# Performance work log

Measured on AMD Instinct MI355X. Metric: run time of the kernel, lower is better.

## Reference

```python
import jax, jax.numpy as jnp
import numpy as np

L, D, H, V, BS = 12, 768, 12, 50257, 1024  # n_layer, n_embd, n_head, vocab, block_size
B, T = 2, 1024
HD = D // H
SCALE = HD ** -0.5


def setup_inputs() -> dict:
    key = jax.random.key(0)
    ks = jax.random.split(key, 10)
    s = 0.02  # init std from _init_weights
    f = lambda k, shape: jax.random.normal(k, shape, jnp.float32) * s
    return {
        "idx": jax.random.randint(ks[0], (B, T), 0, V),
        "tok_emb": f(ks[1], (V, D)),          # tied with LM head
        "pos_emb": f(ks[2], (BS, D)),
        "wqkv": f(ks[3], (L, 3 * D, D)), "bqkv": jnp.zeros((L, 3 * D), jnp.float32),
        "wproj": f(ks[4], (L, D, D)),    "bproj": jnp.zeros((L, D), jnp.float32),
        "ln1_g": jnp.ones((L, D), jnp.float32), "ln1_b": jnp.zeros((L, D), jnp.float32),
        "ln2_g": jnp.ones((L, D), jnp.float32), "ln2_b": jnp.zeros((L, D), jnp.float32),
        "w1": f(ks[5], (L, 4 * D, D)), "b1": jnp.zeros((L, 4 * D), jnp.float32),
        "w2": f(ks[6], (L, D, 4 * D)), "b2": jnp.zeros((L, D), jnp.float32),
        "lnf_g": jnp.ones((D,), jnp.float32), "lnf_b": jnp.zeros((D,), jnp.float32),
    }


def _ln(x, g, b, eps=1e-5):
    mu = jnp.mean(x, axis=-1, keepdims=True)
    var = jnp.mean(jnp.square(x - mu), axis=-1, keepdims=True)
    return (x - mu) * jax.lax.rsqrt(var + eps) * g + b


def _gpt_forward(idx, tok_emb, pos_emb, wqkv, bqkv, wproj, bproj,
                 ln1_g, ln1_b, ln2_g, ln2_b, w1, b1, w2, b2, lnf_g, lnf_b):
    Bb, Tt = idx.shape
    x = tok_emb[idx] + pos_emb[:Tt]  # [B,T,D]; dropout=0 in eval
    causal = jnp.tril(jnp.ones((Tt, Tt), bool))

    def block(x, p):
        wq, bq, wp, bp, g1, be1, g2, be2, W1, B1, W2, B2 = p
        h = _ln(x, g1, be1)
        qkv = h @ wq.T + bq                       # [B,T,3D]
        q, k, v = jnp.split(qkv, 3, axis=-1)
        to_heads = lambda z: z.reshape(Bb, Tt, H, HD).transpose(0, 2, 1, 3)
        q, k, v = to_heads(q), to_heads(k), to_heads(v)
        att = jnp.einsum('bhqd,bhkd->bhqk', q, k) * SCALE
        att = jnp.where(causal, att, -jnp.inf)
        att = jax.nn.softmax(att, axis=-1)
        y = jnp.einsum('bhqk,bhkd->bhqd', att, v)
        y = y.transpose(0, 2, 1, 3).reshape(Bb, Tt, D)
        x = x + (y @ wp.T + bp)
        h2 = _ln(x, g2, be2)
        ff = jax.nn.gelu(h2 @ W1.T + B1, approximate=False) @ W2.T + B2
        return x + ff, None

    layer_params = (wqkv, bqkv, wproj, bproj, ln1_g, ln1_b, ln2_g, ln2_b, w1, b1, w2, b2)
    x, _ = jax.lax.scan(block, x, layer_params)
    x = _ln(x, lnf_g, lnf_b)
    return x @ tok_emb.T  # tied LM head, [B,T,V]


def reference(idx, tok_emb, pos_emb, wqkv, bqkv, wproj, bproj,
              ln1_g, ln1_b, ln2_g, ln2_b, w1, b1, w2, b2, lnf_g, lnf_b):
    return _gpt_forward(idx, tok_emb, pos_emb, wqkv, bqkv, wproj, bproj,
                        ln1_g, ln1_b, ln2_g, ln2_b, w1, b1, w2, b2, lnf_g, lnf_b)
```

## Files before the change

### kernel.cpp

```cpp
#include <hip/hip_runtime.h>
#include <hip/hip_bf16.h>

#define TT 1024
#define DD 768
#define HH 12
#define LL 12
#define VV 50257
#define MROWS 2048

typedef __attribute__((ext_vector_type(4))) float f32x4;
typedef __attribute__((ext_vector_type(8))) short bf16x8;

__device__ __forceinline__ short f2bf(float f) {
  __hip_bfloat16 h = __float2bfloat16(f);
  short s;
  __builtin_memcpy(&s, &h, 2);
  return s;
}

__device__ __forceinline__ void gload16(const void* g, void* l) {
  __builtin_amdgcn_global_load_lds(
      (const __attribute__((address_space(1))) unsigned int*)g,
      (__attribute__((address_space(3))) unsigned int*)l, 16, 0, 0);
}

__device__ __forceinline__ float wsum(float v) {
#pragma unroll
  for (int o = 32; o; o >>= 1) v += __shfl_xor(v, o, 64);
  return v;
}

__global__ __launch_bounds__(256) void cvt_k(const float* __restrict__ src,
                                             short* __restrict__ dst, long n4)
{
  const long stride = (long)gridDim.x * 256;
  for (long i = (long)blockIdx.x * 256 + threadIdx.x; i < n4; i += stride) {
    const float4 v = ((const float4*)src)[i];
    short4 h;
    h.x = f2bf(v.x); h.y = f2bf(v.y); h.z = f2bf(v.z); h.w = f2bf(v.w);
    ((short4*)dst)[i] = h;
  }
}

__global__ __launch_bounds__(256) void embed_k(const int* __restrict__ idx,
    const float* __restrict__ tok, const float* __restrict__ pos,
    float* __restrict__ x)
{
  int i = blockIdx.x * 256 + threadIdx.x;
  int d = i % DD;
  int bt = i / DD;
  int t = bt & (TT - 1);
  x[i] = tok[(long)idx[bt] * DD + d] + pos[t * DD + d];
}

__global__ __launch_bounds__(256) void ln_k(const float* __restrict__ x,
    const float* __restrict__ g, const float* __restrict__ b,
    short* __restrict__ out)
{
  const int row = blockIdx.x;
  const float* xr = x + (long)row * DD;
  float vals[3];
  float s = 0.f, s2 = 0.f;
#pragma unroll
  for (int i = 0; i < 3; ++i) {
    float v = xr[threadIdx.x + i * 256];
    vals[i] = v; s += v; s2 += v * v;
  }
  __shared__ float rs[4], rs2[4];
  s = wsum(s); s2 = wsum(s2);
  if (!(threadIdx.x & 63)) { rs[threadIdx.x >> 6] = s; rs2[threadIdx.x >> 6] = s2; }
  __syncthreads();
  s  = rs[0] + rs[1] + rs[2] + rs[3];
  s2 = rs2[0] + rs2[1] + rs2[2] + rs2[3];
  const float mu = s * (1.f / DD);
  const float var = s2 * (1.f / DD) - mu * mu;
  const float rstd = rsqrtf(var + 1e-5f);
#pragma unroll
  for (int i = 0; i < 3; ++i) {
    int d = threadIdx.x + i * 256;
    out[(long)row * DD + d] = f2bf((vals[i] - mu) * rstd * g[d] + b[d]);
  }
}

__global__ __launch_bounds__(256) void vtrans_k(const short* __restrict__ qkv,
                                                short* __restrict__ vt)
{
  const int tt = blockIdx.x;
  const int z  = blockIdx.y;
  const int zb = z / HH, zh = z % HH;
  __shared__ short tile[64][65];
  for (int e = threadIdx.x; e < 64 * 64; e += 256) {
    int lt = e >> 6, d = e & 63;
    tile[lt][d] = qkv[(long)(zb * TT + tt * 64 + lt) * (3 * DD) + 2 * DD + zh * 64 + d];
  }
  __syncthreads();
  for (int e = threadIdx.x; e < 64 * 64; e += 256) {
    int d = e >> 6, lt = e & 63;
    vt[((long)z * 64 + d) * TT + tt * 64 + lt] = tile[lt][d];
  }
}

__global__ __launch_bounds__(256) void flash_k(const short* __restrict__ qkv,
                                               const short* __restrict__ vt,
                                               short* __restrict__ y)
{
  const int qt = (int)gridDim.x - 1 - (int)blockIdx.x;
  const int z  = blockIdx.y;
  const int zb = z / HH, zh = z % HH;
  const int w    = threadIdx.x >> 6;
  const int lane = threadIdx.x & 63;
  const int c = lane & 15, g = lane >> 4;

  __shared__ short Pl[4][16][40];
  __shared__ float Ol[4][16][64];
  __shared__ float ml[4][16], ll[4][16];

  const int qbase = qt * 16;
  const long rowQ = (long)(zb * TT + qbase + c) * (3 * DD) + zh * 64;

  bf16x8 qf[2];
  qf[0] = *(const bf16x8*)(qkv + rowQ + g * 8);
  qf[1] = *(const bf16x8*)(qkv + rowQ + 32 + g * 8);

  f32x4 O[4] = {};
  f32x4 mrun, lrun;
#pragma unroll
  for (int r = 0; r < 4; ++r) { mrun[r] = -1e30f; lrun[r] = 0.f; }

  const float CSC = 0.125f * 1.44269504089f;
  const int nt = (qbase + 15) / 32 + 1;

  for (int t = w; t < nt; t += 4) {
    const int k0 = t * 32;
    f32x4 acc[2] = {};
#pragma unroll
    for (int nf = 0; nf < 2; ++nf) {
      const long rowK = (long)(zb * TT + k0 + nf * 16 + c) * (3 * DD) + DD + zh * 64;
      bf16x8 kf0 = *(const bf16x8*)(qkv + rowK + g * 8);
      bf16x8 kf1 = *(const bf16x8*)(qkv + rowK + 32 + g * 8);
      acc[nf] = __builtin_amdgcn_mfma_f32_16x16x32_bf16(qf[0], kf0, acc[nf], 0, 0, 0);
      acc[nf] = __builtin_amdgcn_mfma_f32_16x16x32_bf16(qf[1], kf1, acc[nf], 0, 0, 0);
    }
    f32x4 tv[2];
    const int mask_needed = (k0 + 31 > qbase);
#pragma unroll
    for (int nf = 0; nf < 2; ++nf) {
      const int k_abs = k0 + nf * 16 + c;
#pragma unroll
      for (int r = 0; r < 4; ++r) {
        float val = acc[nf][r] * CSC;
        if (mask_needed && k_abs > qbase + g * 4 + r) val = -1e30f;
        tv[nf][r] = val;
      }
    }
    f32x4 rmax;
#pragma unroll
    for (int r = 0; r < 4; ++r) rmax[r] = fmaxf(tv[0][r], tv[1][r]);
#pragma unroll
    for (int off = 1; off < 16; off <<= 1) {
#pragma unroll
      for (int r = 0; r < 4; ++r) rmax[r] = fmaxf(rmax[r], __shfl_xor(rmax[r], off, 64));
    }
    f32x4 mnew, rfac;
#pragma unroll
    for (int r = 0; r < 4; ++r) {
      mnew[r] = fmaxf(mrun[r], rmax[r]);
      rfac[r] = exp2f(mrun[r] - mnew[r]);
      mrun[r] = mnew[r];
    }
    f32x4 e0, e1, rsum;
#pragma unroll
    for (int r = 0; r < 4; ++r) {
      e0[r] = exp2f(tv[0][r] - mnew[r]);
      e1[r] = exp2f(tv[1][r] - mnew[r]);
      rsum[r] = e0[r] + e1[r];
    }
#pragma unroll
    for (int off = 1; off < 16; off <<= 1) {
#pragma unroll
      for (int r = 0; r < 4; ++r) rsum[r] += __shfl_xor(rsum[r], off, 64);
    }
#pragma unroll
    for (int r = 0; r < 4; ++r) lrun[r] = lrun[r] * rfac[r] + rsum[r];
#pragma unroll
    for (int nf = 0; nf < 4; ++nf)
#pragma unroll
      for (int r = 0; r < 4; ++r) O[nf][r] *= rfac[r];
#pragma unroll
    for (int r = 0; r < 4; ++r) {
      Pl[w][g * 4 + r][c]      = f2bf(e0[r]);
      Pl[w][g * 4 + r][16 + c] = f2bf(e1[r]);
    }
    asm volatile("s_waitcnt lgkmcnt(0)" ::: "memory");
    const bf16x8 pf = *(const bf16x8*)&Pl[w][c][g * 8];
#pragma unroll
    for (int nf = 0; nf < 4; ++nf) {
      const bf16x8 vf = *(const bf16x8*)(vt + ((long)z * 64 + nf * 16 + c) * TT + k0 + g * 8);
      O[nf] = __builtin_amdgcn_mfma_f32_16x16x32_bf16(pf, vf, O[nf], 0, 0, 0);
    }
  }

#pragma unroll
  for (int nf = 0; nf < 4; ++nf)
#pragma unroll
    for (int r = 0; r < 4; ++r)
      Ol[w][g * 4 + r][nf * 16 + c] = O[nf][r];
  if (c == 0) {
#pragma unroll
    for (int r = 0; r < 4; ++r) { ml[w][g * 4 + r] = mrun[r]; ll[w][g * 4 + r] = lrun[r]; }
  }
  __syncthreads();

  for (int e = threadIdx.x; e < 16 * 64; e += 256) {
    const int row = e >> 6, d = e & 63;
    const float M = fmaxf(fmaxf(ml[0][row], ml[1][row]), fmaxf(ml[2][row], ml[3][row]));
    float L = 0.f, Ov = 0.f;
#pragma unroll
    for (int u = 0; u < 4; ++u) {
      const float f = exp2f(ml[u][row] - M);
      L += ll[u][row] * f;
      Ov += Ol[u][row][d] * f;
    }
    y[(long)(zb * TT + qbase + row) * DD + zh * 64 + d] = f2bf(Ov / L);
  }
}

template<int BM, int BN, int BK, typename TB, int EPI, bool LMSWZ, bool PIPE>
__global__ __launch_bounds__(256) void gemm_nt(
    const short* __restrict__ A, const TB* __restrict__ Bm,
    const float* __restrict__ bias, const float* __restrict__ resid,
    void* __restrict__ Cout,
    int M, int N, int K, int lda, int ldb, int ldc,
    long aSB, long aSH, long bSB, long bSH, long cSB, long cSH,
    float scale, int causal)
{
  int n0, m0;
  if constexpr (LMSWZ) {
    const int l = blockIdx.x;
    const int x = l & 7;
    const int j = l >> 3;
    const int mt = j & 15;
    const int nl = j >> 4;
    const int npan = (N + BN - 1) / BN;
    const int q = npan >> 3, rr = npan & 7;
    const int cnt = q + (x < rr);
    if (nl >= cnt) return;
    const int nstart = x * q + (x < rr ? x : rr);
    n0 = (nstart + nl) * BN;
    m0 = mt * BM;
  } else {
    n0 = blockIdx.x * BN;
    m0 = blockIdx.y * BM;
  }
  if (causal && n0 >= m0 + BM) return;
  const int z = blockIdx.z;
  const int zb = z / HH, zh = z % HH;
  const short* Ag = A + zb * aSB + zh * aSH + (long)m0 * lda;
  const TB*    Bg = Bm + zb * bSB + zh * bSH;
  const long  cOff = zb * cSB + zh * cSH;

  constexpr int NBUF = PIPE ? 2 : 1;
  __shared__ __align__(16) short Als[NBUF][BM][BK];
  __shared__ __align__(16) short Bls[NBUF][BN][BK];

  const int tid = threadIdx.x;
  const int lane = tid & 63, wid = tid >> 6;
  constexpr int WTM = BM / 2, WTN = BN / 2;
  constexpr int FM = WTM / 16, FN = WTN / 16;
  const int wr = wid >> 1, wc = wid & 1;

  f32x4 acc[FM][FN] = {};
  const int kAoff = (lane >> 4) * 8;
  constexpr bool B_IS_F32 = (sizeof(TB) == 4);
  constexpr int CPR = BK / 8;
  constexpr int NCA = BM * CPR;
  constexpr int NCB = BN * CPR;
  constexpr int IA = NCA / 256, IB = NCB / 256;
  constexpr int GPT = IA + IB;
  static_assert(CPR == 8, "swizzle assumes 128B rows (BK=64)");
  static_assert(B_IS_F32 || (NCA % 256 == 0 && NCB % 256 == 0), "chunk grid");

  auto compute = [&](int buf) {
#pragma unroll
    for (int kk = 0; kk < BK; kk += 32) {
      bf16x8 af[FM], bfr[FN];
#pragma unroll
      for (int mi = 0; mi < FM; ++mi) {
        const int Ra = wr * WTM + mi * 16 + (lane & 15);
        const int kca = (kk + kAoff) >> 3;
        af[mi] = *(const bf16x8*)&Als[buf][Ra][(kca ^ (Ra & 7)) << 3];
      }
#pragma unroll
      for (int ni = 0; ni < FN; ++ni) {
        const int Rb = wc * WTN + ni * 16 + (lane & 15);
        const int kcb = (kk + kAoff) >> 3;
        bfr[ni] = *(const bf16x8*)&Bls[buf][Rb][(kcb ^ (Rb & 7)) << 3];
      }
#pragma unroll
      for (int mi = 0; mi < FM; ++mi)
#pragma unroll
        for (int ni = 0; ni < FN; ++ni)
          acc[mi][ni] = __builtin_amdgcn_mfma_f32_16x16x32_bf16(af[mi], bfr[ni], acc[mi][ni], 0, 0, 0);
    }
  };

  if constexpr (!B_IS_F32) {
    const short* ap[IA];
    const short* bp[IB];
#pragma unroll
    for (int i = 0; i < IA; ++i) {
      const int cch = i * 256 + tid;
      const int r = cch / CPR, kc = cch % CPR;
      ap[i] = Ag + (long)r * lda + ((kc ^ (r & 7)) << 3);
    }
#pragma unroll
    for (int i = 0; i < IB; ++i) {
      const int cch = i * 256 + tid;
      const int r = cch / CPR, kc = cch % CPR;
      int gr = n0 + r; gr = (gr < N) ? gr : (N - 1);
      bp[i] = (const short*)Bg + (long)gr * ldb + ((kc ^ (r & 7)) << 3);
    }
    const int ldsoff = wid * 64 * 16;

    auto stage = [&](int buf) {
#pragma unroll
      for (int i = 0; i < IA; ++i) {
        gload16(ap[i], (char*)&Als[buf][0][0] + i * 4096 + ldsoff);
        ap[i] += BK;
      }
#pragma unroll
      for (int i = 0; i < IB; ++i) {
        gload16(bp[i], (char*)&Bls[buf][0][0] + i * 4096 + ldsoff);
        bp[i] += BK;
      }
    };

    if constexpr (PIPE) {
      const int KT = K / BK;
      stage(0);
      for (int kt = 0; kt < KT; ++kt) {
        const int cur = kt & 1;
        if (kt + 1 < KT) {
          stage(cur ^ 1);
          asm volatile("s_waitcnt vmcnt(%0)" :: "i"(GPT));
        } else {
          asm volatile("s_waitcnt vmcnt(0)");
        }
        __builtin_amdgcn_sched_barrier(0);
        __builtin_amdgcn_s_barrier();
        __builtin_amdgcn_sched_barrier(0);
        compute(cur);
        asm volatile("" ::: "memory");
        __builtin_amdgcn_s_barrier();
        __builtin_amdgcn_sched_barrier(0);
      }
    } else {
      const int KT = K / BK;
      for (int kt = 0; kt < KT; ++kt) {
        stage(0);
        __syncthreads();
        compute(0);
        __syncthreads();
      }
    }
  } else {
    for (int k0 = 0; k0 < K; k0 += BK) {
#pragma unroll
      for (int cc = tid; cc < BM * (BK / 8); cc += 256) {
        int r = cc / (BK / 8), kc = cc % (BK / 8);
        const uint4 v = *(const uint4*)(Ag + (long)r * lda + k0 + kc * 8);
        *(uint4*)((char*)&Als[0][r][0] + ((kc ^ (r & 7)) << 4)) = v;
      }
#pragma unroll
      for (int cc = tid; cc < BN * (BK / 4); cc += 256) {
        int r = cc / (BK / 4), kc = cc % (BK / 4);
        int gr = n0 + r; gr = (gr < N) ? gr : (N - 1);
        const float4 v = *(const float4*)((const float*)Bg + (long)gr * ldb + k0 + kc * 4);
        short4 h4;
        h4.x = f2bf(v.x); h4.y = f2bf(v.y); h4.z = f2bf(v.z); h4.w = f2bf(v.w);
        *(short4*)((char*)&Bls[0][r][0] + ((kc * 8) ^ ((r & 7) << 4))) = h4;
      }
      __syncthreads();
      compute(0);
      __syncthreads();
    }
  }

  const int rq = (lane >> 4) << 2;
  const int cl = lane & 15;
#pragma unroll
  for (int mi = 0; mi < FM; ++mi) {
#pragma unroll
    for (int ni = 0; ni < FN; ++ni) {
      const int cg = n0 + wc * WTN + ni * 16 + cl;
      if (cg >= N) continue;
      const int rbase = m0 + wr * WTM + mi * 16 + rq;
#pragma unroll
      for (int q = 0; q < 4; ++q) {
        const long cidx = cOff + (long)(rbase + q) * ldc + cg;
        const float v = acc[mi][ni][q];
        if constexpr (EPI == 0) {
          ((float*)Cout)[cidx] = v * scale;
        } else if constexpr (EPI == 1) {
          ((short*)Cout)[cidx] = f2bf(v + bias[cg]);
        } else if constexpr (EPI == 2) {
          ((float*)Cout)[cidx] = resid[cidx] + v + bias[cg];
        } else if constexpr (EPI == 3) {
          const float zz = v + bias[cg];
          ((short*)Cout)[cidx] = f2bf(0.5f * zz * (1.f + erff(zz * 0.70710678118f)));
        } else {
          ((short*)Cout)[cidx] = f2bf(v);
        }
      }
    }
  }
}

template<typename TB>
static void run_model(const int* idx, const float* tok_f, const float* pos,
                      const TB* wqkv, const float* bqkv, const TB* wproj, const float* bproj,
                      const float* ln1g, const float* ln1b, const float* ln2g, const float* ln2b,
                      const TB* w1, const float* b1, const TB* w2, const float* b2,
                      const float* lnfg, const float* lnfb, const TB* tok_w,
                      float* xa, float* xb, short* hbf, short* qkv, short* vt,
                      short* ybf, short* ffb,
                      float* out, hipStream_t stream)
{
  embed_k<<<dim3(MROWS * DD / 256), 256, 0, stream>>>(idx, tok_f, pos, xa);

  float* xc = xa;
  float* xn = xb;
  for (int l = 0; l < LL; ++l) {
    ln_k<<<dim3(MROWS), 256, 0, stream>>>(xc, ln1g + l * DD, ln1b + l * DD, hbf);
    gemm_nt<128, 64, 64, TB, 1, false, true><<<dim3(36, 16, 1), 256, 0, stream>>>(
        hbf, wqkv + (long)l * 3 * DD * DD, bqkv + l * 3 * DD, nullptr, qkv,
        MROWS, 3 * DD, DD, DD, DD, 3 * DD, 0, 0, 0, 0, 0, 0, 1.f, 0);
    vtrans_k<<<dim3(16, 24), 256, 0, stream>>>(qkv, vt);
    flash_k<<<dim3(64, 24), 256, 0, stream>>>(qkv, vt, ybf);
    gemm_nt<64, 64, 64, TB, 2, false, true><<<dim3(12, 32, 1), 256, 0, stream>>>(
        ybf, wproj + (long)l * DD * DD, bproj + l * DD, xc, xn,
        MROWS, DD, DD, DD, DD, DD, 0, 0, 0, 0, 0, 0, 1.f, 0);
    ln_k<<<dim3(MROWS), 256, 0, stream>>>(xn, ln2g + l * DD, ln2b + l * DD, hbf);
    gemm_nt<128, 64, 64, TB, 3, false, true><<<dim3(48, 16, 1), 256, 0, stream>>>(
        hbf, w1 + (long)l * 4 * DD * DD, b1 + l * 4 * DD, nullptr, ffb,
        MROWS, 4 * DD, DD, DD, DD, 4 * DD, 0, 0, 0, 0, 0, 0, 1.f, 0);
    gemm_nt<64, 64, 64, TB, 2, false, true><<<dim3(12, 32, 1), 256, 0, stream>>>(
        ffb, w2 + (long)l * DD * 4 * DD, b2 + l * DD, xn, xc,
        MROWS, DD, 4 * DD, 4 * DD, 4 * DD, DD, 0, 0, 0, 0, 0, 0, 1.f, 0);
  }
  ln_k<<<dim3(MROWS), 256, 0, stream>>>(xc, lnfg, lnfb, hbf);
  gemm_nt<128, 128, 64, TB, 0, true, false><<<dim3(6400, 1, 1), 256, 0, stream>>>(
      hbf, tok_w, nullptr, nullptr, out,
      MROWS, VV, DD, DD, DD, VV, 0, 0, 0, 0, 0, 0, 1.f, 0);
}

extern "C" void kernel_launch(void* const* d_in, const int* in_sizes, int n_in,
                              void* d_out, int out_size, void* d_ws, size_t ws_size,
                              hipStream_t stream)
{
  const int*   idx  = (const int*)d_in[0];
  const float* tok  = (const float*)d_in[1];
  const float* pos  = (const float*)d_in[2];
  const float* wqkv = (const float*)d_in[3];
  const float* bqkv = (const float*)d_in[4];
  const float* wproj= (const float*)d_in[5];
  const float* bproj= (const float*)d_in[6];
  const float* ln1g = (const float*)d_in[7];
  const float* ln1b = (const float*)d_in[8];
  const float* ln2g = (const float*)d_in[9];
  const float* ln2b = (const float*)d_in[10];
  const float* w1   = (const float*)d_in[11];
  const float* b1   = (const float*)d_in[12];
  const float* w2   = (const float*)d_in[13];
  const float* b2   = (const float*)d_in[14];
  const float* lnfg = (const float*)d_in[15];
  const float* lnfb = (const float*)d_in[16];
  float* out = (float*)d_out;

  const long E_WQKV = (long)LL * 3 * DD * DD;
  const long E_WPRJ = (long)LL * DD * DD;
  const long E_W1   = (long)LL * 4 * DD * DD;
  const long E_W2   = E_W1;
  const long E_TOK  = (long)VV * DD;
  const long E_WSUM = E_WQKV + E_WPRJ + E_W1 + E_W2 + E_TOK;

  const size_t NEED_B = 44040192;
  const size_t NEED_A = NEED_B + 2 * (size_t)E_WSUM;

  if (ws_size < NEED_B) return;
  const bool bf16w = (ws_size >= NEED_A);

  char* ws = (char*)d_ws;
  short *wqkv_h = nullptr, *wprj_h = nullptr, *w1_h = nullptr, *w2_h = nullptr, *tok_h = nullptr;
  if (bf16w) {
    wqkv_h = (short*)ws; ws += E_WQKV * 2;
    wprj_h = (short*)ws; ws += E_WPRJ * 2;
    w1_h   = (short*)ws; ws += E_W1 * 2;
    w2_h   = (short*)ws; ws += E_W2 * 2;
    tok_h  = (short*)ws; ws += E_TOK * 2;
  }
  float* xa  = (float*)ws; ws += (size_t)MROWS * DD * 4;
  float* xb  = (float*)ws; ws += (size_t)MROWS * DD * 4;
  short* hbf = (short*)ws; ws += (size_t)MROWS * DD * 2;
  short* qkv = (short*)ws; ws += (size_t)MROWS * 3 * DD * 2;
  short* vt  = (short*)ws; ws += (size_t)24 * 64 * TT * 2;
  short* ybf = (short*)ws; ws += (size_t)MROWS * DD * 2;
  short* ffb = (short*)ws; ws += (size_t)MROWS * 4 * DD * 2;

  if (bf16w) {
    cvt_k<<<dim3(2048), 256, 0, stream>>>(wqkv, wqkv_h, E_WQKV / 4);
    cvt_k<<<dim3(2048), 256, 0, stream>>>(wproj, wprj_h, E_WPRJ / 4);
    cvt_k<<<dim3(2048), 256, 0, stream>>>(w1, w1_h, E_W1 / 4);
    cvt_k<<<dim3(2048), 256, 0, stream>>>(w2, w2_h, E_W2 / 4);
    cvt_k<<<dim3(2048), 256, 0, stream>>>(tok, tok_h, E_TOK / 4);
    run_model<short>(idx, tok, pos, wqkv_h, bqkv, wprj_h, bproj,
                     ln1g, ln1b, ln2g, ln2b, w1_h, b1, w2_h, b2, lnfg, lnfb, tok_h,
                     xa, xb, hbf, qkv, vt, ybf, ffb, out, stream);
  } else {
    run_model<float>(idx, tok, pos, wqkv, bqkv, wproj, bproj,
                     ln1g, ln1b, ln2g, ln2b, w1, b1, w2, b2, lnfg, lnfb, tok,
                     xa, xb, hbf, qkv, vt, ybf, ffb, out, stream);
  }
}
```

Measured before the change: 2.275 ms.

## Add M-replication to GEMM tiles and enlarge per-layer GEMM tile sizes

Adds an MREP template parameter so each block computes several BM-row sub-tiles against one staged B tile. This reuses B fragments from LDS across sub-tiles and halves the block count of the LM-head GEMM. The per-layer QKV, FC1, proj and FC2 GEMMs also move to larger N tiles (128 or 96), giving fewer blocks and more reuse per block. The cost is more accumulator registers and LDS, and fewer blocks, which may lower occupancy and leave CUs idle on the smaller GEMMs.

```diff
diff --git a/kernel.cpp b/kernel.cpp
--- a/kernel.cpp
+++ b/kernel.cpp
@@ -225,7 +225,7 @@
   }
 }
 
-template<int BM, int BN, int BK, typename TB, int EPI, bool LMSWZ, bool PIPE>
+template<int BM, int BN, int BK, int MREP, typename TB, int EPI, bool LMSWZ, bool PIPE>
 __global__ __launch_bounds__(256) void gemm_nt(
     const short* __restrict__ A, const TB* __restrict__ Bm,
     const float* __restrict__ bias, const float* __restrict__ resid,
@@ -239,20 +239,20 @@
     const int l = blockIdx.x;
     const int x = l & 7;
     const int j = l >> 3;
-    const int mt = j & 15;
-    const int nl = j >> 4;
+    const int mt = j & 7;
+    const int nl = j >> 3;
     const int npan = (N + BN - 1) / BN;
     const int q = npan >> 3, rr = npan & 7;
     const int cnt = q + (x < rr);
     if (nl >= cnt) return;
     const int nstart = x * q + (x < rr ? x : rr);
     n0 = (nstart + nl) * BN;
-    m0 = mt * BM;
+    m0 = mt * (BM * MREP);
   } else {
     n0 = blockIdx.x * BN;
-    m0 = blockIdx.y * BM;
-  }
-  if (causal && n0 >= m0 + BM) return;
+    m0 = blockIdx.y * (BM * MREP);
+  }
+  if (causal && n0 >= m0 + BM * MREP) return;
   const int z = blockIdx.z;
   const int zb = z / HH, zh = z % HH;
   const short* Ag = A + zb * aSB + zh * aSH + (long)m0 * lda;
@@ -260,7 +260,8 @@
   const long  cOff = zb * cSB + zh * cSH;
 
   constexpr int NBUF = PIPE ? 2 : 1;
-  __shared__ __align__(16) short Als[NBUF][BM][BK];
+  constexpr int AR = BM * MREP;
+  __shared__ __align__(16) short Als[NBUF][AR][BK];
   __shared__ __align__(16) short Bls[NBUF][BN][BK];
 
   const int tid = threadIdx.x;
@@ -269,11 +270,11 @@
   constexpr int FM = WTM / 16, FN = WTN / 16;
   const int wr = wid >> 1, wc = wid & 1;
 
-  f32x4 acc[FM][FN] = {};
+  f32x4 acc[MREP][FM][FN] = {};
   const int kAoff = (lane >> 4) * 8;
   constexpr bool B_IS_F32 = (sizeof(TB) == 4);
   constexpr int CPR = BK / 8;
-  constexpr int NCA = BM * CPR;
+  constexpr int NCA = AR * CPR;
   constexpr int NCB = BN * CPR;
   constexpr int IA = NCA / 256, IB = NCB / 256;
   constexpr int GPT = IA + IB;
@@ -283,24 +284,27 @@
   auto compute = [&](int buf) {
 #pragma unroll
     for (int kk = 0; kk < BK; kk += 32) {
-      bf16x8 af[FM], bfr[FN];
-#pragma unroll
-      for (int mi = 0; mi < FM; ++mi) {
-        const int Ra = wr * WTM + mi * 16 + (lane & 15);
-        const int kca = (kk + kAoff) >> 3;
-        af[mi] = *(const bf16x8*)&Als[buf][Ra][(kca ^ (Ra & 7)) << 3];
-      }
+      const int kc = (kk + kAoff) >> 3;
+      bf16x8 bfr[FN];
 #pragma unroll
       for (int ni = 0; ni < FN; ++ni) {
         const int Rb = wc * WTN + ni * 16 + (lane & 15);
-        const int kcb = (kk + kAoff) >> 3;
-        bfr[ni] = *(const bf16x8*)&Bls[buf][Rb][(kcb ^ (Rb & 7)) << 3];
-      }
-#pragma unroll
-      for (int mi = 0; mi < FM; ++mi)
-#pragma unroll
-        for (int ni = 0; ni < FN; ++ni)
-          acc[mi][ni] = __builtin_amdgcn_mfma_f32_16x16x32_bf16(af[mi], bfr[ni], acc[mi][ni], 0, 0, 0);
+        bfr[ni] = *(const bf16x8*)&Bls[buf][Rb][(kc ^ (Rb & 7)) << 3];
+      }
+#pragma unroll
+      for (int mp = 0; mp < MREP; ++mp) {
+        bf16x8 af[FM];
+#pragma unroll
+        for (int mi = 0; mi < FM; ++mi) {
+          const int Ra = mp * BM + wr * WTM + mi * 16 + (lane & 15);
+          af[mi] = *(const bf16x8*)&Als[buf][Ra][(kc ^ (Ra & 7)) << 3];
+        }
+#pragma unroll
+        for (int mi = 0; mi < FM; ++mi)
+#pragma unroll
+          for (int ni = 0; ni < FN; ++ni)
+            acc[mp][mi][ni] = __builtin_amdgcn_mfma_f32_16x16x32_bf16(af[mi], bfr[ni], acc[mp][mi][ni], 0, 0, 0);
+      }
     }
   };
 
@@ -366,8 +370,8 @@
   } else {
     for (int k0 = 0; k0 < K; k0 += BK) {
 #pragma unroll
-      for (int cc = tid; cc < BM * (BK / 8); cc += 256) {
-        int r = cc / (BK / 8), kc = cc % (BK / 8);
+      for (int cc = tid; cc < NCA; cc += 256) {
+        int r = cc / CPR, kc = cc % CPR;
         const uint4 v = *(const uint4*)(Ag + (long)r * lda + k0 + kc * 8);
         *(uint4*)((char*)&Als[0][r][0] + ((kc ^ (r & 7)) << 4)) = v;
       }
@@ -389,27 +393,30 @@
   const int rq = (lane >> 4) << 2;
   const int cl = lane & 15;
 #pragma unroll
-  for (int mi = 0; mi < FM; ++mi) {
-#pragma unroll
-    for (int ni = 0; ni < FN; ++ni) {
-      const int cg = n0 + wc * WTN + ni * 16 + cl;
-      if (cg >= N) continue;
-      const int rbase = m0 + wr * WTM + mi * 16 + rq;
-#pragma unroll
-      for (int q = 0; q < 4; ++q) {
-        const long cidx = cOff + (long)(rbase + q) * ldc + cg;
-        const float v = acc[mi][ni][q];
-        if constexpr (EPI == 0) {
-          ((float*)Cout)[cidx] = v * scale;
-        } else if constexpr (EPI == 1) {
-          ((short*)Cout)[cidx] = f2bf(v + bias[cg]);
-        } else if constexpr (EPI == 2) {
-          ((float*)Cout)[cidx] = resid[cidx] + v + bias[cg];
-        } else if constexpr (EPI == 3) {
-          const float zz = v + bias[cg];
-          ((short*)Cout)[cidx] = f2bf(0.5f * zz * (1.f + erff(zz * 0.70710678118f)));
-        } else {
-          ((short*)Cout)[cidx] = f2bf(v);
+  for (int mp = 0; mp < MREP; ++mp) {
+#pragma unroll
+    for (int mi = 0; mi < FM; ++mi) {
+#pragma unroll
+      for (int ni = 0; ni < FN; ++ni) {
+        const int cg = n0 + wc * WTN + ni * 16 + cl;
+        if (cg >= N) continue;
+        const int rbase = m0 + mp * BM + wr * WTM + mi * 16 + rq;
+#pragma unroll
+        for (int q = 0; q < 4; ++q) {
+          const long cidx = cOff + (long)(rbase + q) * ldc + cg;
+          const float v = acc[mp][mi][ni][q];
+          if constexpr (EPI == 0) {
+            ((float*)Cout)[cidx] = v * scale;
+          } else if constexpr (EPI == 1) {
+            ((short*)Cout)[cidx] = f2bf(v + bias[cg]);
+          } else if constexpr (EPI == 2) {
+            ((float*)Cout)[cidx] = resid[cidx] + v + bias[cg];
+          } else if constexpr (EPI == 3) {
+            const float zz = v + bias[cg];
+            ((short*)Cout)[cidx] = f2bf(0.5f * zz * (1.f + erff(zz * 0.70710678118f)));
+          } else {
+            ((short*)Cout)[cidx] = f2bf(v);
+          }
         }
       }
     }
@@ -432,24 +439,24 @@
   float* xn = xb;
   for (int l = 0; l < LL; ++l) {
     ln_k<<<dim3(MROWS), 256, 0, stream>>>(xc, ln1g + l * DD, ln1b + l * DD, hbf);
-    gemm_nt<128, 64, 64, TB, 1, false, true><<<dim3(36, 16, 1), 256, 0, stream>>>(
+    gemm_nt<128, 128, 64, 1, TB, 1, false, true><<<dim3(18, 16, 1), 256, 0, stream>>>(
         hbf, wqkv + (long)l * 3 * DD * DD, bqkv + l * 3 * DD, nullptr, qkv,
         MROWS, 3 * DD, DD, DD, DD, 3 * DD, 0, 0, 0, 0, 0, 0, 1.f, 0);
     vtrans_k<<<dim3(16, 24), 256, 0, stream>>>(qkv, vt);
     flash_k<<<dim3(64, 24), 256, 0, stream>>>(qkv, vt, ybf);
-    gemm_nt<64, 64, 64, TB, 2, false, true><<<dim3(12, 32, 1), 256, 0, stream>>>(
+    gemm_nt<64, 96, 64, 1, TB, 2, false, true><<<dim3(8, 32, 1), 256, 0, stream>>>(
         ybf, wproj + (long)l * DD * DD, bproj + l * DD, xc, xn,
         MROWS, DD, DD, DD, DD, DD, 0, 0, 0, 0, 0, 0, 1.f, 0);
     ln_k<<<dim3(MROWS), 256, 0, stream>>>(xn, ln2g + l * DD, ln2b + l * DD, hbf);
-    gemm_nt<128, 64, 64, TB, 3, false, true><<<dim3(48, 16, 1), 256, 0, stream>>>(
+    gemm_nt<128, 128, 64, 1, TB, 3, false, true><<<dim3(24, 16, 1), 256, 0, stream>>>(
         hbf, w1 + (long)l * 4 * DD * DD, b1 + l * 4 * DD, nullptr, ffb,
         MROWS, 4 * DD, DD, DD, DD, 4 * DD, 0, 0, 0, 0, 0, 0, 1.f, 0);
-    gemm_nt<64, 64, 64, TB, 2, false, true><<<dim3(12, 32, 1), 256, 0, stream>>>(
+    gemm_nt<64, 96, 64, 1, TB, 2, false, true><<<dim3(8, 32, 1), 256, 0, stream>>>(
         ffb, w2 + (long)l * DD * 4 * DD, b2 + l * DD, xn, xc,
         MROWS, DD, 4 * DD, 4 * DD, 4 * DD, DD, 0, 0, 0, 0, 0, 0, 1.f, 0);
   }
   ln_k<<<dim3(MROWS), 256, 0, stream>>>(xc, lnfg, lnfb, hbf);
-  gemm_nt<128, 128, 64, TB, 0, true, false><<<dim3(6400, 1, 1), 256, 0, stream>>>(
+  gemm_nt<128, 128, 64, 2, TB, 0, true, false><<<dim3(3200, 1, 1), 256, 0, stream>>>(
       hbf, tok_w, nullptr, nullptr, out,
       MROWS, VV, DD, DD, DD, VV, 0, 0, 0, 0, 0, 0, 1.f, 0);
 }
```

Measured after the change: 2.694 ms. +18.4%, slower.
